# Kernel tuning notes

Hardware: AMD Instinct MI355X
Metric: run time of the kernel (lower is better)

Reference implementation:

```python
import jax, jax.numpy as jnp
import numpy as np

B, K, NPROP, NSAMPLE = 16, 2048, 256, 16
C_SEED, C_MLP = 256, 128
RADIUS = 0.3
NH, NSC, NCLS = 12, 18, 18
KZ, KXY, KLINE = 1024, 1024, 1024
SURF_TH, UP_TH = 0.5, 10.0
OUT_CH = 2 + 3 + 2 * NH + 4 * NSC + NCLS  # 119


def setup_inputs():
    key = jax.random.key(0)
    ks = iter(jax.random.split(key, 64))
    nrm = lambda shape, sc=1.0: sc * jax.random.normal(next(ks), shape, jnp.float32)
    uni = lambda shape: jax.random.uniform(next(ks), shape, jnp.float32, minval=-2.0, maxval=2.0)
    inp = {
        'vote_xyz': uni((B, K, 3)),
        'vote_features': nrm((B, C_SEED, K)),
        'pred_sem_class_z': nrm((B, 2, KZ)),
        'center_z': uni((B, KZ, 3)),
        'aggregated_feature_z': nrm((B, 128, KZ)),
        'pred_sem_class_xy': nrm((B, 2, KXY)),
        'center_xy': uni((B, KXY, 3)),
        'aggregated_feature_xy': nrm((B, 128, KXY)),
        'pred_sem_class_line': nrm((B, 2, KLINE)),
        'center_line': uni((B, KLINE, 3)),
        'aggregated_feature_line': nrm((B, 128, KLINE)),
        'mean_size_arr': jnp.abs(nrm((NSC, 3))) * 0.5 + 0.3,
        'mlp_w0': nrm((C_MLP, C_SEED + 3), 0.05),
        'mlp_s0': 1.0 + nrm((C_MLP,), 0.02),
        'mlp_b0': nrm((C_MLP,), 0.02),
        'mlp_w1': nrm((C_MLP, C_MLP), 0.05),
        'mlp_s1': 1.0 + nrm((C_MLP,), 0.02),
        'mlp_b1': nrm((C_MLP,), 0.02),
        'mlp_w2': nrm((C_MLP, C_MLP), 0.05),
        'mlp_s2': 1.0 + nrm((C_MLP,), 0.02),
        'mlp_b2': nrm((C_MLP,), 0.02),
        'conv1_w': nrm((C_MLP, C_MLP), 0.05),
        'conv1_b': nrm((C_MLP,), 0.02),
        'bn1_s': 1.0 + nrm((C_MLP,), 0.02),
        'bn1_b': nrm((C_MLP,), 0.02),
        'conv2_w': nrm((C_MLP, C_MLP), 0.05),
        'conv2_b': nrm((C_MLP,), 0.02),
        'bn2_s': 1.0 + nrm((C_MLP,), 0.02),
        'bn2_b': nrm((C_MLP,), 0.02),
        'conv3_w': nrm((OUT_CH, C_MLP), 0.05),
        'conv3_b': nrm((OUT_CH,), 0.02),
    }
    return inp


def fps(xyz, npoint):
    # furthest point sampling; xyz (B,N,3) -> (B,npoint) int32
    Bn, N, _ = xyz.shape
    bidx = jnp.arange(Bn)

    def step(carry, _):
        dist, far = carry
        centroid = xyz[bidx, far][:, None, :]  # (B,1,3)
        d = jnp.sum((xyz - centroid) ** 2, -1)
        dist = jnp.minimum(dist, d)
        nxt = jnp.argmax(dist, -1).astype(jnp.int32)
        return (dist, nxt), far

    init = (jnp.full((Bn, N), 1e10, xyz.dtype), jnp.zeros((Bn,), jnp.int32))
    _, inds = jax.lax.scan(step, init, None, length=npoint)
    return inds.T


def ball_group(xyz, feat_t, new_xyz, radius, nsample):
    # first-nsample-in-ball semantics (as CUDA ball_query), pad with first hit
    Bn, N, _ = xyz.shape
    d2 = jnp.sum((new_xyz[:, :, None] - xyz[:, None]) ** 2, -1)  # (B,P,N)
    score = jnp.where(d2 <= radius * radius, jnp.arange(N, dtype=jnp.int32), N)
    neg, idx = jax.lax.top_k(-score, nsample)
    idx = jnp.where(-neg < N, idx, idx[..., :1])
    b = jnp.arange(Bn)[:, None, None]
    gx = (xyz[b, idx] - new_xyz[:, :, None]) / radius  # normalize_xyz=True
    gf = feat_t[b, idx]
    return jnp.concatenate([gx, gf], -1)  # (B,P,ns,3+C)


def reference(vote_xyz, vote_features, pred_sem_class_z, center_z, aggregated_feature_z,
              pred_sem_class_xy, center_xy, aggregated_feature_xy,
              pred_sem_class_line, center_line, aggregated_feature_line, mean_size_arr,
              mlp_w0, mlp_s0, mlp_b0, mlp_w1, mlp_s1, mlp_b1, mlp_w2, mlp_s2, mlp_b2,
              conv1_w, conv1_b, bn1_s, bn1_b, conv2_w, conv2_b, bn2_s, bn2_b, conv3_w, conv3_b):
    # --- vote aggregation (PointnetSAModuleVotes, vote_fps) ---
    fps_inds = fps(vote_xyz, NPROP)
    bi = jnp.arange(vote_xyz.shape[0])[:, None]
    new_xyz = vote_xyz[bi, fps_inds]  # (B,P,3)
    g = ball_group(vote_xyz, vote_features.transpose(0, 2, 1), new_xyz, RADIUS, NSAMPLE)
    for w, s, b in ((mlp_w0, mlp_s0, mlp_b0), (mlp_w1, mlp_s1, mlp_b1), (mlp_w2, mlp_s2, mlp_b2)):
        g = jax.nn.relu(jnp.einsum('bpsc,oc->bpso', g, w) * s + b)  # conv2d 1x1 + folded BN + relu
    features = g.max(axis=2).transpose(0, 2, 1)  # (B,128,P)

    c1d = lambda x, w, b: jnp.einsum('bck,oc->bok', x, w) + b[None, :, None]
    bn = lambda x, s, b: x * s[None, :, None] + b[None, :, None]

    net = jax.nn.relu(bn(c1d(features, conv1_w, conv1_b), bn1_s, bn1_b))
    net = jax.nn.relu(bn(c1d(net, conv2_w, conv2_b), bn2_s, bn2_b))
    net = c1d(net, conv3_w, conv3_b)  # (B,119,P)

    # --- decode_scores (mode='center', start=2) ---
    nt = net.transpose(0, 2, 1)
    Bn, P = nt.shape[0], nt.shape[1]
    objectness = nt[..., 0:2]
    center = new_xyz + nt[..., 2:5]
    heading_scores = nt[..., 5:5 + NH]
    heading_res = nt[..., 5 + NH:5 + 2 * NH] * (np.pi / NH)
    size_scores = nt[..., 5 + 2 * NH:5 + 2 * NH + NSC]
    srn = nt[..., 5 + 2 * NH + NSC:5 + 2 * NH + 4 * NSC].reshape(Bn, P, NSC, 3)
    size_res = srn * mean_size_arr[None, None]
    sem_cls = nt[..., 5 + 2 * NH + 4 * NSC:]

    # --- surface / line center selection ---
    def sel_center(pred_sem, c):
        p = jax.nn.softmax(pred_sem, axis=1)
        sel = jax.lax.stop_gradient((p[:, 1, :] <= SURF_TH).astype(c.dtype))
        return c + UP_TH * sel[..., None]

    z_center = sel_center(pred_sem_class_z, center_z)
    xy_center = sel_center(pred_sem_class_xy, center_xy)
    line_center = sel_center(pred_sem_class_line, center_line)
    surface_center_pred = jnp.concatenate([z_center, xy_center], axis=1)
    surface_center_feature_pred = jnp.concatenate([aggregated_feature_z, aggregated_feature_xy], axis=2)

    # --- predicted box size -> 6 object surface centers ---
    cls = jnp.argmax(size_scores, -1)  # (B,P)
    pred_res = jnp.take_along_axis(size_res, cls[..., None, None], axis=2)[:, :, 0]
    pred_avg = mean_size_arr[cls]
    obj_size = jax.lax.stop_gradient(pred_avg + pred_res)  # .detach() in torch
    half = obj_size / 2.0
    z0 = jnp.zeros_like(half[..., :1])
    ez = jnp.concatenate([z0, z0, half[..., 2:3]], -1)
    ey = jnp.concatenate([z0, half[..., 1:2], z0], -1)
    ex = jnp.concatenate([half[..., 0:1], z0, z0], -1)
    obj_surface_center = jnp.concatenate([center + ez, center - ez, center + ey,
                                          center - ey, center + ex, center - ex], axis=1)
    obj_surface_feature = jnp.tile(features, (1, 1, 6))

    return (objectness, center, heading_scores, heading_res, size_scores, size_res, sem_cls,
            surface_center_pred, surface_center_feature_pred, line_center,
            obj_surface_center, obj_surface_feature)
```

## Files before the change

### kernel.cpp

```cpp
#include <hip/hip_runtime.h>

#define BB 16
#define KK 2048
#define NPROPN 256
#define NS 16
#define CSEED 256
#define CMLP 128
#define CIN 259
#define OUTCH 119
#define KZZ 1024

#define O0  0UL
#define O1  8192UL
#define O2  20480UL
#define O3  69632UL
#define O4  118784UL
#define O5  192512UL
#define O6  413696UL
#define O7  487424UL
#define O8  585728UL
#define O9  4780032UL
#define O10 4829184UL
#define O11 4902912UL

#define WS_NEWXYZ 0
#define WS_W0T 12288
#define WS_W1T 45440
#define WS_W2T 61824
#define WS_C1T 78208
#define WS_C2T 94592
#define WS_C3T 110976
#define WS_FEATT 131072UL
#define WS_NEED_BYTES ((size_t)(WS_FEATT + (size_t)BB * KK * CSEED) * 4)

#define XROWS 131
#define XSTR (XROWS * 16)

#define RSTEP(CTRL)                                                                          \
  {                                                                                          \
    unsigned shi = (unsigned)__builtin_amdgcn_update_dpp((int)hi, (int)hi, (CTRL), 0xF, 0xF, false); \
    unsigned slo = (unsigned)__builtin_amdgcn_update_dpp((int)lo, (int)lo, (CTRL), 0xF, 0xF, false); \
    bool gt = (shi > hi) || ((shi == hi) && (slo > lo));                                     \
    hi = gt ? shi : hi;                                                                      \
    lo = gt ? slo : lo;                                                                      \
  }

__device__ __forceinline__ void fma4(float4& a, float s, const float4& w) {
  a.x = fmaf(s, w.x, a.x); a.y = fmaf(s, w.y, a.y);
  a.z = fmaf(s, w.z, a.z); a.w = fmaf(s, w.w, a.w);
}
__device__ __forceinline__ float fget(const float4& v, int r) {
  return r == 0 ? v.x : (r == 1 ? v.y : (r == 2 ? v.z : v.w));
}
__device__ __forceinline__ int xadr(int row, int s4) {
  return row * 16 + (((s4) ^ ((row >> 2) & 3)) << 2);
}

template<bool TR>
__global__ __launch_bounds__(256) void prep_kernel(
    const float* __restrict__ xyz, const float* __restrict__ vote_feat,
    const float* __restrict__ w0, const float* __restrict__ w1, const float* __restrict__ w2,
    const float* __restrict__ c1w, const float* __restrict__ c2w, const float* __restrict__ c3w,
    const float* __restrict__ pz, const float* __restrict__ cz,
    const float* __restrict__ pxy, const float* __restrict__ cxy,
    const float* __restrict__ pl, const float* __restrict__ cl,
    const float* __restrict__ az, const float* __restrict__ axy,
    float* __restrict__ wsf, float* __restrict__ out) {
  constexpr int FPS_END = 16;
  constexpr int FEATT_END = FPS_END + (TR ? 1024 : 0);
  constexpr int TRW_END = FEATT_END + 450;
  constexpr int SURF_END = TRW_END + 192;

  const int bid = blockIdx.x;
  const int t = threadIdx.x;
  __shared__ float smem[8448];
  __shared__ float wvv[2][4];
  __shared__ int wii[2][4];

  if (bid < FPS_END) {
    const int b = bid;
    const float* p = xyz + (size_t)b * KK * 3;
    float* sxyz = smem;
    float* nxb = smem + 6144;
    const int lane = t & 63, w = t >> 6;
    float pxr[8], pyr[8], pzr[8], dd[8];
#pragma unroll
    for (int j = 0; j < 8; ++j) {
      int i = j * 256 + t;
      float x = p[i * 3 + 0], y = p[i * 3 + 1], z = p[i * 3 + 2];
      pxr[j] = x; pyr[j] = y; pzr[j] = z; dd[j] = 1e10f;
      sxyz[i * 3 + 0] = x; sxyz[i * 3 + 1] = y; sxyz[i * 3 + 2] = z;
    }
    __syncthreads();
    int cur = 0;
    for (int it = 0; it < NPROPN; ++it) {
      const int pb = it & 1;
      float cx = sxyz[cur * 3 + 0];
      float cy = sxyz[cur * 3 + 1];
      float cz2 = sxyz[cur * 3 + 2];
      if (t == 0) { nxb[it * 3 + 0] = cx; nxb[it * 3 + 1] = cy; nxb[it * 3 + 2] = cz2; }
      float best = -1.0f;
      int bidx = 0;
#pragma unroll
      for (int j = 0; j < 8; ++j) {
        float dx = __fsub_rn(pxr[j], cx);
        float dy = __fsub_rn(pyr[j], cy);
        float dz = __fsub_rn(pzr[j], cz2);
        float d = __fadd_rn(__fadd_rn(__fmul_rn(dx, dx), __fmul_rn(dy, dy)), __fmul_rn(dz, dz));
        float nd = fminf(dd[j], d);
        dd[j] = nd;
        if (nd > best) { best = nd; bidx = j * 256 + t; }
      }
      unsigned hi = __float_as_uint(best);
      unsigned lo = ~(unsigned)bidx;
      RSTEP(0x111) RSTEP(0x112) RSTEP(0x114) RSTEP(0x118)
      RSTEP(0x142) RSTEP(0x143)
      if (lane == 63) { wvv[pb][w] = __uint_as_float(hi); wii[pb][w] = (int)lo; }
      __syncthreads();
      unsigned vh = __float_as_uint(wvv[pb][0]);
      unsigned vl = (unsigned)wii[pb][0];
#pragma unroll
      for (int q2 = 1; q2 < 4; ++q2) {
        unsigned ah = __float_as_uint(wvv[pb][q2]);
        unsigned al = (unsigned)wii[pb][q2];
        bool gt = (ah > vh) || ((ah == vh) && (al > vl));
        vh = gt ? ah : vh; vl = gt ? al : vl;
      }
      cur = (int)~vl;
    }
    __syncthreads();
    float* nxw = wsf + WS_NEWXYZ + (size_t)b * NPROPN * 3;
    for (int i = t; i < NPROPN * 3; i += 256) nxw[i] = nxb[i];
    return;
  }

  if (TR && bid < FEATT_END) {
    int q = bid - FPS_END;
    int b = q >> 6, ck = q & 63;
    int k0 = ck << 5;
    float* tile = smem;
    const float* src = vote_feat + ((size_t)b * CSEED + t) * KK + k0;
    float4 v[8];
#pragma unroll
    for (int j = 0; j < 8; ++j) v[j] = *(const float4*)(src + j * 4);
#pragma unroll
    for (int j = 0; j < 8; ++j) {
      tile[(j * 4 + 0) * 260 + t] = v[j].x;
      tile[(j * 4 + 1) * 260 + t] = v[j].y;
      tile[(j * 4 + 2) * 260 + t] = v[j].z;
      tile[(j * 4 + 3) * 260 + t] = v[j].w;
    }
    __syncthreads();
    float* dst = wsf + WS_FEATT + ((size_t)b * KK + k0) * CSEED;
    const int kk = t >> 3, cbase = (t & 7) << 2;
#pragma unroll
    for (int j = 0; j < 8; ++j) {
      int c = cbase + (j << 5);
      float4 u = make_float4(tile[kk * 260 + c], tile[kk * 260 + c + 1],
                             tile[kk * 260 + c + 2], tile[kk * 260 + c + 3]);
      *(float4*)(dst + (size_t)kk * CSEED + c) = u;
    }
    return;
  }

  if (bid < TRW_END) {
    int row = (bid - FEATT_END) * 2 + (t >> 7);
    int o = t & 127;
    if (row < 899) {
      float v; float* dst;
      if (row < 259)      { dst = wsf + WS_W0T + (size_t)row * 128; v = w0[(size_t)o * CIN + row]; }
      else if (row < 387) { int k = row - 259; dst = wsf + WS_W1T + (size_t)k * 128; v = w1[(size_t)o * 128 + k]; }
      else if (row < 515) { int k = row - 387; dst = wsf + WS_W2T + (size_t)k * 128; v = w2[(size_t)o * 128 + k]; }
      else if (row < 643) { int k = row - 515; dst = wsf + WS_C1T + (size_t)k * 128; v = c1w[(size_t)o * 128 + k]; }
      else if (row < 771) { int k = row - 643; dst = wsf + WS_C2T + (size_t)k * 128; v = c2w[(size_t)o * 128 + k]; }
      else                { int k = row - 771; dst = wsf + WS_C3T + (size_t)k * 128; v = (o < OUTCH) ? c3w[(size_t)o * 128 + k] : 0.f; }
      dst[o] = v;
    }
    return;
  }

  if (bid < SURF_END) {
    int i = (bid - TRW_END) * 256 + t;
    int src = i / (BB * KZZ);
    int rem = i % (BB * KZZ);
    int b = rem / KZZ, k = rem % KZZ;
    const float* ps = (src == 0) ? pz : ((src == 1) ? pxy : pl);
    const float* pc = (src == 0) ? cz : ((src == 1) ? cxy : cl);
    float x0 = ps[((size_t)b * 2 + 0) * KZZ + k];
    float x1 = ps[((size_t)b * 2 + 1) * KZZ + k];
    float add = (x1 <= x0) ? 10.0f : 0.0f;
    size_t dst;
    if (src == 0)      dst = O7 + ((size_t)b * 2048 + k) * 3;
    else if (src == 1) dst = O7 + ((size_t)b * 2048 + 1024 + k) * 3;
    else               dst = O9 + ((size_t)b * KZZ + k) * 3;
    const float* c3 = pc + ((size_t)b * KZZ + k) * 3;
    out[dst + 0] = c3[0] + add;
    out[dst + 1] = c3[1] + add;
    out[dst + 2] = c3[2] + add;
    return;
  }

  {
    int i = (bid - SURF_END) * 256 + t;
    int q = i & 511;
    int bc = i >> 9;
    int half = q >> 8, k4 = q & 255;
    const float4* src = (const float4*)((half == 0) ? az : axy);
    float4 v = src[(size_t)bc * 256 + k4];
    float4* dst = (float4*)(out + O8);
    dst[(size_t)bc * 512 + q] = v;
  }
}

__device__ __forceinline__ void mlp_accum(const float* __restrict__ WT, int og, int sh,
                                          const float* __restrict__ xb, int K, float4* acc) {
  const float4* wp = (const float4*)WT + og;
  const int s4a = sh * 2, s4b = sh * 2 + 1;
#pragma unroll 4
  for (int k = 0; k < K; ++k) {
    float4 xa = *(const float4*)(xb + xadr(k, s4a));
    float4 xq = *(const float4*)(xb + xadr(k, s4b));
    float4 wv = wp[(size_t)k * 32];
    fma4(acc[0], xa.x, wv); fma4(acc[1], xa.y, wv);
    fma4(acc[2], xa.z, wv); fma4(acc[3], xa.w, wv);
    fma4(acc[4], xq.x, wv); fma4(acc[5], xq.y, wv);
    fma4(acc[6], xq.z, wv); fma4(acc[7], xq.w, wv);
  }
}

__device__ __forceinline__ void mlp_storeh(const float* __restrict__ scv, const float* __restrict__ bbv,
                                           int og, int sh, float* __restrict__ xb,
                                           const float4* __restrict__ acc) {
  float4 s4v = *(const float4*)(scv + (og << 2));
  float4 b4v = *(const float4*)(bbv + (og << 2));
#pragma unroll
  for (int r = 0; r < 4; ++r) {
    float ss = fget(s4v, r), bv = fget(b4v, r);
    float4 lo, hi;
    lo.x = fmaf(fget(acc[0], r), ss, bv); lo.x = lo.x > 0.f ? lo.x : 0.f;
    lo.y = fmaf(fget(acc[1], r), ss, bv); lo.y = lo.y > 0.f ? lo.y : 0.f;
    lo.z = fmaf(fget(acc[2], r), ss, bv); lo.z = lo.z > 0.f ? lo.z : 0.f;
    lo.w = fmaf(fget(acc[3], r), ss, bv); lo.w = lo.w > 0.f ? lo.w : 0.f;
    hi.x = fmaf(fget(acc[4], r), ss, bv); hi.x = hi.x > 0.f ? hi.x : 0.f;
    hi.y = fmaf(fget(acc[5], r), ss, bv); hi.y = hi.y > 0.f ? hi.y : 0.f;
    hi.z = fmaf(fget(acc[6], r), ss, bv); hi.z = hi.z > 0.f ? hi.z : 0.f;
    hi.w = fmaf(fget(acc[7], r), ss, bv); hi.w = hi.w > 0.f ? hi.w : 0.f;
    int row = (og << 2) + r;
    *(float4*)(xb + xadr(row, sh * 2)) = lo;
    *(float4*)(xb + xadr(row, sh * 2 + 1)) = hi;
  }
}

template<bool TR>
__global__ __launch_bounds__(256, 4) void proposal_kernel(
    const float* __restrict__ vote_xyz, const float* __restrict__ vote_feat,
    const float* __restrict__ wsf, const float* __restrict__ msa,
    const float* __restrict__ s0, const float* __restrict__ b0,
    const float* __restrict__ s1, const float* __restrict__ b1,
    const float* __restrict__ s2, const float* __restrict__ b2,
    const float* __restrict__ c1b, const float* __restrict__ bn1s, const float* __restrict__ bn1b,
    const float* __restrict__ c2b, const float* __restrict__ bn2s, const float* __restrict__ bn2b,
    const float* __restrict__ c3b,
    float* __restrict__ out) {
  __shared__ __align__(16) float Xbuf[4 * XSTR];
  __shared__ int sel_s[4][NS];
  __shared__ float sc_s[4][3], sh_s[4][3];
  __shared__ int scls_s[4];

  const int t = threadIdx.x;
  const int w = t >> 6, l = t & 63;
  const int b = blockIdx.x >> 6;
  const int pp = ((blockIdx.x & 63) << 2) + w;
  const int sh = l >> 5, og = l & 31;
  float* Xw = Xbuf + w * XSTR;
  float* feat_p = Xw;
  float* n1_p   = Xw + 128;
  float* n2_p   = Xw + 256;
  float* ntv_p  = Xw + 384;

  const float* nx = wsf + WS_NEWXYZ + ((size_t)b * NPROPN + pp) * 3;
  const float cx = nx[0], cy = nx[1], cz = nx[2];
  const float* px = vote_xyz + (size_t)b * KK * 3;
  const float RR = 0.09000000357627869f;

  {
    int total = 0;
    for (int j0 = 0; j0 < 32 && total < NS; j0 += 8) {
      float dq[8];
#pragma unroll
      for (int jj = 0; jj < 8; ++jj) {
        int i = ((j0 + jj) << 6) + l;
        float dx = __fsub_rn(px[i * 3 + 0], cx);
        float dy = __fsub_rn(px[i * 3 + 1], cy);
        float dz = __fsub_rn(px[i * 3 + 2], cz);
        dq[jj] = __fadd_rn(__fadd_rn(__fmul_rn(dx, dx), __fmul_rn(dy, dy)), __fmul_rn(dz, dz));
      }
#pragma unroll
      for (int jj = 0; jj < 8; ++jj) {
        bool in = (dq[jj] <= RR);
        unsigned long long bal = __ballot(in);
        if (in) {
          int pos = total + __popcll(bal & ((1ull << l) - 1ull));
          if (pos < NS) sel_s[w][pos] = ((j0 + jj) << 6) + l;
        }
        total += __popcll(bal);
      }
    }
    if (l == 0 && total < NS) {
      int first = (total > 0) ? sel_s[w][0] : 0;
      for (int i = total; i < NS; ++i) sel_s[w][i] = first;
    }
    __builtin_amdgcn_wave_barrier();
  }

  float4 pf[8];
  {
    const int s = l >> 2, q = l & 3;
    const int idx = sel_s[w][s];
    const int s4 = s >> 2, se = s & 3;
    if (q < 3) {
      float pv = px[idx * 3 + q];
      float cv = (q == 0) ? cx : ((q == 1) ? cy : cz);
      Xw[xadr(q, s4) + se] = __fdiv_rn(__fsub_rn(pv, cv), 0.3f);
    }
    if constexpr (TR) {
      const float* fr = wsf + WS_FEATT + ((size_t)b * KK + idx) * CSEED;
#pragma unroll
      for (int m = 0; m < 8; ++m) {
        int c = (m << 4) + (q << 2);
        float4 v = *(const float4*)(fr + c);
        Xw[xadr(3 + c + 0, s4) + se] = v.x;
        Xw[xadr(3 + c + 1, s4) + se] = v.y;
        Xw[xadr(3 + c + 2, s4) + se] = v.z;
        Xw[xadr(3 + c + 3, s4) + se] = v.w;
      }
#pragma unroll
      for (int m = 0; m < 8; ++m) pf[m] = *(const float4*)(fr + 128 + (m << 4) + (q << 2));
    } else {
      const float* fb = vote_feat + (size_t)b * CSEED * KK + idx;
#pragma unroll
      for (int m = 0; m < 8; ++m) {
        int c = (m << 4) + (q << 2);
        Xw[xadr(3 + c + 0, s4) + se] = fb[(size_t)(c + 0) * KK];
        Xw[xadr(3 + c + 1, s4) + se] = fb[(size_t)(c + 1) * KK];
        Xw[xadr(3 + c + 2, s4) + se] = fb[(size_t)(c + 2) * KK];
        Xw[xadr(3 + c + 3, s4) + se] = fb[(size_t)(c + 3) * KK];
      }
#pragma unroll
      for (int m = 0; m < 8; ++m) {
        int c = 128 + (m << 4) + (q << 2);
        pf[m].x = fb[(size_t)(c + 0) * KK];
        pf[m].y = fb[(size_t)(c + 1) * KK];
        pf[m].z = fb[(size_t)(c + 2) * KK];
        pf[m].w = fb[(size_t)(c + 3) * KK];
      }
    }
    __builtin_amdgcn_wave_barrier();
  }

  float4 acc[8];
#pragma unroll
  for (int i = 0; i < 8; ++i) acc[i] = make_float4(0.f, 0.f, 0.f, 0.f);

  mlp_accum(wsf + WS_W0T, og, sh, Xw, 131, acc);
  __builtin_amdgcn_wave_barrier();

  {
    const int s = l >> 2, q = l & 3;
    const int s4 = s >> 2, se = s & 3;
#pragma unroll
    for (int m = 0; m < 8; ++m) {
      int c = (m << 4) + (q << 2);
      Xw[xadr(c + 0, s4) + se] = pf[m].x;
      Xw[xadr(c + 1, s4) + se] = pf[m].y;
      Xw[xadr(c + 2, s4) + se] = pf[m].z;
      Xw[xadr(c + 3, s4) + se] = pf[m].w;
    }
    __builtin_amdgcn_wave_barrier();
  }

  mlp_accum(wsf + WS_W0T + 131 * 128, og, sh, Xw, 128, acc);
  mlp_storeh(s0, b0, og, sh, Xw, acc);
  __builtin_amdgcn_wave_barrier();

#pragma unroll
  for (int i = 0; i < 8; ++i) acc[i] = make_float4(0.f, 0.f, 0.f, 0.f);
  mlp_accum(wsf + WS_W1T, og, sh, Xw, 128, acc);
  mlp_storeh(s1, b1, og, sh, Xw, acc);
  __builtin_amdgcn_wave_barrier();

#pragma unroll
  for (int i = 0; i < 8; ++i) acc[i] = make_float4(0.f, 0.f, 0.f, 0.f);
  mlp_accum(wsf + WS_W2T, og, sh, Xw, 128, acc);

  float mr[4];
  {
    float4 s4v = *(const float4*)(s2 + (og << 2));
    float4 b4v = *(const float4*)(b2 + (og << 2));
#pragma unroll
    for (int r = 0; r < 4; ++r) {
      float ss = fget(s4v, r), bv = fget(b4v, r);
      float m = 0.f;
#pragma unroll
      for (int i = 0; i < 8; ++i) m = fmaxf(m, fmaf(fget(acc[i], r), ss, bv));
      mr[r] = fmaxf(m, __shfl_xor(m, 32));
    }
  }
  __builtin_amdgcn_wave_barrier();
  if (sh == 0) *(float4*)(feat_p + (og << 2)) = make_float4(mr[0], mr[1], mr[2], mr[3]);
  __builtin_amdgcn_wave_barrier();

  {
    float* o11 = out + O11 + (size_t)b * CMLP * 1536;
#pragma unroll
    for (int r = 0; r < 4; ++r) {
      size_t rowb = (size_t)((og << 2) + r) * 1536 + pp;
#pragma unroll
      for (int rr2 = 0; rr2 < 3; ++rr2) {
        int rr = sh * 3 + rr2;
        o11[rowb + rr * 256] = mr[r];
      }
    }
  }

  {
    const float* C1T = wsf + WS_C1T;
    float a0 = 0.f, a1 = 0.f;
#pragma unroll 4
    for (int k = 0; k < CMLP; ++k) {
      float f = feat_p[k];
      float2 wv = *(const float2*)(C1T + (size_t)k * 128 + (l << 1));
      a0 = fmaf(f, wv.x, a0); a1 = fmaf(f, wv.y, a1);
    }
    int o0 = l << 1, o1 = o0 + 1;
    float v0 = fmaf(a0 + c1b[o0], bn1s[o0], bn1b[o0]); v0 = v0 > 0.f ? v0 : 0.f;
    float v1 = fmaf(a1 + c1b[o1], bn1s[o1], bn1b[o1]); v1 = v1 > 0.f ? v1 : 0.f;
    *(float2*)(n1_p + o0) = make_float2(v0, v1);
    __builtin_amdgcn_wave_barrier();
  }
  {
    const float* C2T = wsf + WS_C2T;
    float a0 = 0.f, a1 = 0.f;
#pragma unroll 4
    for (int k = 0; k < CMLP; ++k) {
      float f = n1_p[k];
      float2 wv = *(const float2*)(C2T + (size_t)k * 128 + (l << 1));
      a0 = fmaf(f, wv.x, a0); a1 = fmaf(f, wv.y, a1);
    }
    int o0 = l << 1, o1 = o0 + 1;
    float v0 = fmaf(a0 + c2b[o0], bn2s[o0], bn2b[o0]); v0 = v0 > 0.f ? v0 : 0.f;
    float v1 = fmaf(a1 + c2b[o1], bn2s[o1], bn2b[o1]); v1 = v1 > 0.f ? v1 : 0.f;
    *(float2*)(n2_p + o0) = make_float2(v0, v1);
    __builtin_amdgcn_wave_barrier();
  }
  {
    const float* C3T = wsf + WS_C3T;
    float a0 = 0.f, a1 = 0.f;
#pragma unroll 4
    for (int k = 0; k < CMLP; ++k) {
      float f = n2_p[k];
      float2 wv = *(const float2*)(C3T + (size_t)k * 128 + (l << 1));
      a0 = fmaf(f, wv.x, a0); a1 = fmaf(f, wv.y, a1);
    }
    int o0 = l << 1, o1 = o0 + 1;
    float bb0 = (o0 < OUTCH) ? c3b[o0] : 0.f;
    float bb1 = (o1 < OUTCH) ? c3b[o1] : 0.f;
    *(float2*)(ntv_p + o0) = make_float2(a0 + bb0, a1 + bb1);
    __builtin_amdgcn_wave_barrier();
  }

  {
    const size_t bp = (size_t)b * NPROPN + pp;
    if (l < 2) out[O0 + bp * 2 + l] = ntv_p[l];
    if (l < 3) {
      float cv = ((l == 0) ? cx : ((l == 1) ? cy : cz)) + ntv_p[2 + l];
      sc_s[w][l] = cv;
      out[O1 + bp * 3 + l] = cv;
    }
    if (l < 12) {
      out[O2 + bp * 12 + l] = ntv_p[5 + l];
      out[O3 + bp * 12 + l] = ntv_p[17 + l] * 0.2617993877991494f;
    }
    if (l < 18) {
      out[O4 + bp * 18 + l] = ntv_p[29 + l];
      out[O6 + bp * 18 + l] = ntv_p[101 + l];
    }
    if (l < 54) out[O5 + bp * 54 + l] = ntv_p[47 + l] * msa[l];
    if (l == 0) {
      float bvv = ntv_p[29]; int bii = 0;
      for (int i2 = 1; i2 < 18; ++i2)
        if (ntv_p[29 + i2] > bvv) { bvv = ntv_p[29 + i2]; bii = i2; }
      scls_s[w] = bii;
    }
    __builtin_amdgcn_wave_barrier();
    if (l < 3) {
      int cls = scls_s[w];
      float m = msa[cls * 3 + l];
      sh_s[w][l] = fmaf(ntv_p[47 + cls * 3 + l], m, m) * 0.5f;
    }
    __builtin_amdgcn_wave_barrier();
    if (l < 18) {
      const int r = l / 3, j2 = l % 3;
      const int axis[6] = {2, 2, 1, 1, 0, 0};
      float v = sc_s[w][j2];
      if (j2 == axis[r]) v = (r & 1) ? (v - sh_s[w][j2]) : (v + sh_s[w][j2]);
      out[O10 + (size_t)b * 4608 + (size_t)(r * 256 + pp) * 3 + j2] = v;
    }
  }
}

extern "C" void kernel_launch(void* const* d_in, const int* in_sizes, int n_in,
                              void* d_out, int out_size, void* d_ws, size_t ws_size,
                              hipStream_t stream) {
  (void)in_sizes; (void)n_in; (void)out_size;
  const float* vote_xyz = (const float*)d_in[0];
  const float* vote_feat = (const float*)d_in[1];
  const float* pz   = (const float*)d_in[2];
  const float* cz   = (const float*)d_in[3];
  const float* az   = (const float*)d_in[4];
  const float* pxy  = (const float*)d_in[5];
  const float* cxy  = (const float*)d_in[6];
  const float* axy  = (const float*)d_in[7];
  const float* pl   = (const float*)d_in[8];
  const float* cl   = (const float*)d_in[9];
  const float* msa  = (const float*)d_in[11];
  const float* w0   = (const float*)d_in[12];
  const float* s0   = (const float*)d_in[13];
  const float* b0   = (const float*)d_in[14];
  const float* w1   = (const float*)d_in[15];
  const float* s1   = (const float*)d_in[16];
  const float* b1   = (const float*)d_in[17];
  const float* w2   = (const float*)d_in[18];
  const float* s2   = (const float*)d_in[19];
  const float* b2   = (const float*)d_in[20];
  const float* c1w  = (const float*)d_in[21];
  const float* c1b  = (const float*)d_in[22];
  const float* bn1s = (const float*)d_in[23];
  const float* bn1b = (const float*)d_in[24];
  const float* c2w  = (const float*)d_in[25];
  const float* c2b  = (const float*)d_in[26];
  const float* bn2s = (const float*)d_in[27];
  const float* bn2b = (const float*)d_in[28];
  const float* c3w  = (const float*)d_in[29];
  const float* c3b  = (const float*)d_in[30];
  float* out = (float*)d_out;
  float* wsf = (float*)d_ws;

  if (ws_size >= WS_NEED_BYTES) {
    hipLaunchKernelGGL((prep_kernel<true>), dim3(16 + 1024 + 450 + 192 + 4096), dim3(256), 0, stream,
                       vote_xyz, vote_feat, w0, w1, w2, c1w, c2w, c3w,
                       pz, cz, pxy, cxy, pl, cl, az, axy, wsf, out);
    hipLaunchKernelGGL((proposal_kernel<true>), dim3(BB * NPROPN / 4), dim3(256), 0, stream,
                       vote_xyz, vote_feat, wsf, msa,
                       s0, b0, s1, b1, s2, b2,
                       c1b, bn1s, bn1b, c2b, bn2s, bn2b, c3b, out);
  } else {
    hipLaunchKernelGGL((prep_kernel<false>), dim3(16 + 450 + 192 + 4096), dim3(256), 0, stream,
                       vote_xyz, vote_feat, w0, w1, w2, c1w, c2w, c3w,
                       pz, cz, pxy, cxy, pl, cl, az, axy, wsf, out);
    hipLaunchKernelGGL((proposal_kernel<false>), dim3(BB * NPROPN / 4), dim3(256), 0, stream,
                       vote_xyz, vote_feat, wsf, msa,
                       s0, b0, s1, b1, s2, b2,
                       c1b, bn1s, bn1b, c2b, bn2s, bn2b, c3b, out);
  }
}
```

Baseline: 329.5 us.

## Split MLP K-dimension across wave halves when few neighbours found

When a proposal's ball query finds at most 8 neighbours, only samples 0-7 (the distinct ones) matter. In that case the two half-waves split the reduction dimension between them instead of each computing a separate set of 8 samples, and the partial sums are then combined with cross-lane shuffles. This roughly halves the serial FMA loop length for sparse proposals, at the cost of extra shuffles, a clamped tail iteration and a divergent code path. Correctness relies on samples 8-15 duplicating earlier ones when fewer than 9 points are found, which keeps the max-pool unchanged.

```diff
diff --git a/kernel.cpp b/kernel.cpp
--- a/kernel.cpp
+++ b/kernel.cpp
@@ -228,6 +228,35 @@
   }
 }
 
+__device__ __forceinline__ void mlp_accum_pair(const float* __restrict__ WT, int og, int sh,
+                                               const float* __restrict__ xb, int K, float4* acc) {
+  const float4* wp = (const float4*)WT + og;
+#pragma unroll 4
+  for (int k2 = 0; k2 < K; k2 += 2) {
+    int myk = k2 + sh;
+    int mk = myk < K ? myk : (K - 1);
+    float4 xa = *(const float4*)(xb + xadr(mk, 0));
+    float4 xq = *(const float4*)(xb + xadr(mk, 1));
+    float4 wv = wp[(size_t)mk * 32];
+    if (myk < K) {
+      fma4(acc[0], xa.x, wv); fma4(acc[1], xa.y, wv);
+      fma4(acc[2], xa.z, wv); fma4(acc[3], xa.w, wv);
+      fma4(acc[4], xq.x, wv); fma4(acc[5], xq.y, wv);
+      fma4(acc[6], xq.z, wv); fma4(acc[7], xq.w, wv);
+    }
+  }
+}
+
+__device__ __forceinline__ void pair_combine(float4* acc) {
+#pragma unroll
+  for (int i = 0; i < 8; ++i) {
+    acc[i].x += __shfl_xor(acc[i].x, 32);
+    acc[i].y += __shfl_xor(acc[i].y, 32);
+    acc[i].z += __shfl_xor(acc[i].z, 32);
+    acc[i].w += __shfl_xor(acc[i].w, 32);
+  }
+}
+
 __device__ __forceinline__ void mlp_storeh(const float* __restrict__ scv, const float* __restrict__ bbv,
                                            int og, int sh, float* __restrict__ xb,
                                            const float4* __restrict__ acc) {
@@ -283,8 +312,8 @@
   const float* px = vote_xyz + (size_t)b * KK * 3;
   const float RR = 0.09000000357627869f;
 
-  {
-    int total = 0;
+  int total = 0;
+  {
     for (int j0 = 0; j0 < 32 && total < NS; j0 += 8) {
       float dq[8];
 #pragma unroll
@@ -358,14 +387,7 @@
     __builtin_amdgcn_wave_barrier();
   }
 
-  float4 acc[8];
-#pragma unroll
-  for (int i = 0; i < 8; ++i) acc[i] = make_float4(0.f, 0.f, 0.f, 0.f);
-
-  mlp_accum(wsf + WS_W0T, og, sh, Xw, 131, acc);
-  __builtin_amdgcn_wave_barrier();
-
-  {
+  auto write_chunk1 = [&]() {
     const int s = l >> 2, q = l & 3;
     const int s4 = s >> 2, se = s & 3;
 #pragma unroll
@@ -376,22 +398,48 @@
       Xw[xadr(c + 2, s4) + se] = pf[m].z;
       Xw[xadr(c + 3, s4) + se] = pf[m].w;
     }
-    __builtin_amdgcn_wave_barrier();
-  }
-
-  mlp_accum(wsf + WS_W0T + 131 * 128, og, sh, Xw, 128, acc);
-  mlp_storeh(s0, b0, og, sh, Xw, acc);
-  __builtin_amdgcn_wave_barrier();
-
+  };
+
+  float4 acc[8];
 #pragma unroll
   for (int i = 0; i < 8; ++i) acc[i] = make_float4(0.f, 0.f, 0.f, 0.f);
-  mlp_accum(wsf + WS_W1T, og, sh, Xw, 128, acc);
-  mlp_storeh(s1, b1, og, sh, Xw, acc);
-  __builtin_amdgcn_wave_barrier();
-
-#pragma unroll
-  for (int i = 0; i < 8; ++i) acc[i] = make_float4(0.f, 0.f, 0.f, 0.f);
-  mlp_accum(wsf + WS_W2T, og, sh, Xw, 128, acc);
+
+  if (total <= 8) {
+    mlp_accum_pair(wsf + WS_W0T, og, sh, Xw, 131, acc);
+    __builtin_amdgcn_wave_barrier();
+    write_chunk1();
+    __builtin_amdgcn_wave_barrier();
+    mlp_accum_pair(wsf + WS_W0T + 131 * 128, og, sh, Xw, 128, acc);
+    pair_combine(acc);
+    mlp_storeh(s0, b0, og, sh, Xw, acc);
+    __builtin_amdgcn_wave_barrier();
+#pragma unroll
+    for (int i = 0; i < 8; ++i) acc[i] = make_float4(0.f, 0.f, 0.f, 0.f);
+    mlp_accum_pair(wsf + WS_W1T, og, sh, Xw, 128, acc);
+    pair_combine(acc);
+    mlp_storeh(s1, b1, og, sh, Xw, acc);
+    __builtin_amdgcn_wave_barrier();
+#pragma unroll
+    for (int i = 0; i < 8; ++i) acc[i] = make_float4(0.f, 0.f, 0.f, 0.f);
+    mlp_accum_pair(wsf + WS_W2T, og, sh, Xw, 128, acc);
+    pair_combine(acc);
+  } else {
+    mlp_accum(wsf + WS_W0T, og, sh, Xw, 131, acc);
+    __builtin_amdgcn_wave_barrier();
+    write_chunk1();
+    __builtin_amdgcn_wave_barrier();
+    mlp_accum(wsf + WS_W0T + 131 * 128, og, sh, Xw, 128, acc);
+    mlp_storeh(s0, b0, og, sh, Xw, acc);
+    __builtin_amdgcn_wave_barrier();
+#pragma unroll
+    for (int i = 0; i < 8; ++i) acc[i] = make_float4(0.f, 0.f, 0.f, 0.f);
+    mlp_accum(wsf + WS_W1T, og, sh, Xw, 128, acc);
+    mlp_storeh(s1, b1, og, sh, Xw, acc);
+    __builtin_amdgcn_wave_barrier();
+#pragma unroll
+    for (int i = 0; i < 8; ++i) acc[i] = make_float4(0.f, 0.f, 0.f, 0.f);
+    mlp_accum(wsf + WS_W2T, og, sh, Xw, 128, acc);
+  }
 
   float mr[4];
   {
```

New measurement: 326.3 us. About the same (-1.0%).
